# Kernel optimization log

Hardware: AMD Instinct MI355X
Metric: run time of the kernel (lower is better)

## Reference

```python
import jax, jax.numpy as jnp
import numpy as np

N, T = 4096, 1024
COND, PRED, PERIOD = 896, 56, 7


def setup_inputs() -> dict:
    key = jax.random.key(0)
    k1, k2 = jax.random.split(key)
    query = jax.random.normal(k1, (N, T), dtype=jnp.float32)
    # learned per-location params: [init_level, level_sm_logit, init_trend,
    #  trend_sm_logit, season_sm, period seasonality logits]
    params = 0.1 * jax.random.normal(k2, (N, 5 + PERIOD), dtype=jnp.float32)
    return {"query": query, "params": params}


def _forward(query, params):
    init_level = params[:, 0]                       # [N]
    level_sm = jax.nn.sigmoid(params[:, 1])         # [N]
    init_trend = params[:, 2]                       # [N]
    trend_sm = jax.nn.sigmoid(params[:, 3])         # [N]
    season_sm = params[:, 4]                        # NOTE: no sigmoid, matches original code
    init_seas = jax.nn.sigmoid(params[:, -PERIOD:])  # [N, PERIOD]

    def step(carry, y):
        prev_level, prev_trend, buf = carry          # buf: rolling window of last PERIOD seasonalities
        s_t = buf[:, 0]                              # seasonalities[t]
        pred = prev_level + prev_trend
        level = level_sm * y + (1.0 - level_sm) * pred
        diff = jnp.abs(level - prev_level)
        trend = trend_sm * (level - prev_level) + (1.0 - trend_sm) * prev_trend
        new_seas = season_sm * (y - pred) + (1.0 - season_sm) * s_t
        buf = jnp.concatenate([buf[:, 1:], new_seas[:, None]], axis=1)
        return (level, trend, buf), (level, trend, new_seas, diff)

    carry0 = (init_level, init_trend, init_seas)
    _, (levels, trends, new_seas_seq, diffs) = jax.lax.scan(step, carry0, query.T)
    levels = levels.T            # [N, T]
    trends = trends.T            # [N, T]
    new_seas_seq = new_seas_seq.T  # [N, T], == seasonalities[:, PERIOD:]
    level_diffs = diffs.T.mean(axis=1)  # [N]

    # full seasonality sequence: PERIOD initial values followed by T computed ones
    seas_full = jnp.concatenate([init_seas, new_seas_seq], axis=1)  # [N, PERIOD+T]

    sm = query - levels - new_seas_seq  # [N, T]

    horizon = jnp.arange(1, PRED + 1, dtype=levels.dtype)  # [PRED]
    last_levels = levels[:, COND - 1:, None]   # [N, W, 1], W = T-COND+1
    last_trends = trends[:, COND - 1:, None]
    pr = last_levels + last_trends * horizon   # [N, W, PRED]

    # cyclic seasonality forecast per window
    season_index = jnp.tile(jnp.arange(PERIOD), (PRED + PERIOD - 1) // PERIOD)[:PRED]
    starts = jnp.arange(COND, T + 1)           # [W]
    idx = starts[:, None] + season_index[None, :]  # [W, PRED]
    pr = pr + seas_full[:, idx]                # [N, W, PRED]

    return sm, pr, level_diffs


def reference(query, params):
    return _forward(query, params)
```

## Files before the change

kernel.cpp:

```cpp
#include <hip/hip_runtime.h>
#include <cmath>

#define NROWS 4096
#define TLEN  1024
#define RPB   8
#define LT0   895
#define ST0   889
#define LTN   129
#define STN   135
#define PRV4R 1806
#define PRV4B (RPB * PRV4R)

__device__ __forceinline__ float sigmoidf_(float x) {
    return 1.0f / (1.0f + expf(-x));
}

__device__ __forceinline__ float f4c(const float4& v, int k) {
    switch (k & 3) { case 0: return v.x; case 1: return v.y; case 2: return v.z; default: return v.w; }
}

__global__ __launch_bounds__(512, 4)
void es_fused(const float* __restrict__ query,
              const float* __restrict__ params,
              float* __restrict__ sm,
              float* __restrict__ diffs,
              float4* __restrict__ pr4)
{
    __shared__ float4 ystage[RPB * 256];
    __shared__ float lds_P[RPB * 65];
    __shared__ float lds_start[RPB * 65];
    __shared__ float lds_q[RPB * 225];
    __shared__ float lds_dsum[RPB * 33];
    __shared__ float lds_par[RPB * 16];
    __shared__ float Ltl[RPB * 132];
    __shared__ float Ttl[RPB * 132];
    __shared__ float Stl[RPB * 136];

    const int tid = threadIdx.x;
    const int base = blockIdx.x * RPB;
    const int r = (tid >> 5) & 7;
    const int k = tid & 31;
    const int n = base + r;

    {
        const float4* qb = reinterpret_cast<const float4*>(query + (size_t)base * TLEN);
        #pragma unroll
        for (int i = 0; i < 4; ++i) {
            const int w = i * 512 + tid;
            ystage[(w & ~7) | ((w ^ (w >> 3)) & 7)] = qb[w];
        }
    }

    float a = 0.f, b = 0.f, c = 0.f, ia = 0.f, ib = 0.f, ic = 0.f;
    if (tid < 256) {
        const float* pp = params + (size_t)n * 12;
        a  = sigmoidf_(pp[1]);
        b  = sigmoidf_(pp[3]);
        c  = pp[4];
        ia = 1.0f - a; ib = 1.0f - b; ic = 1.0f - c;
        if (k == 0) {
            float* par = &lds_par[r * 16];
            par[0] = pp[0];
            par[1] = pp[2];
            par[2] = ia;
            par[3] = -(a * b);
            par[4] = ib + b * ia;
            par[5] = ic;
            #pragma unroll
            for (int l = 0; l < 7; ++l) par[6 + l] = sigmoidf_(pp[5 + l]);
        }
    }
    __syncthreads();

    float4 yv[8];
    float e[32];
    float st0 = 0.f, st1 = 0.f;

    if (tid < 256) {
        const int ksw = k & 7;
        #pragma unroll
        for (int i = 0; i < 8; ++i)
            yv[i] = ystage[r * 256 + ((k * 8 + i) ^ ksw)];

        float L = 0.0f, B = 0.0f;
        #pragma unroll
        for (int j = 0; j < 32; ++j) {
            const float yy = f4c(yv[j >> 2], j);
            const float pred  = L + B;
            const float level = fmaf(a, yy, ia * pred);
            const float trend = fmaf(b, level - L, ib * B);
            L = level; B = trend;
        }
        lds_P[r * 65 + 2 * k]     = L;
        lds_P[r * 65 + 2 * k + 1] = B;
    }
    __syncthreads();

    if (tid < 8) {
        const float* par = &lds_par[tid * 16];
        float m00 = par[2], m01 = par[2], m10 = par[3], m11 = par[4];
        #pragma unroll
        for (int s = 0; s < 5; ++s) {
            const float t00 = m00 * m00 + m01 * m10;
            const float t01 = m00 * m01 + m01 * m11;
            const float t10 = m10 * m00 + m11 * m10;
            const float t11 = m10 * m01 + m11 * m11;
            m00 = t00; m01 = t01; m10 = t10; m11 = t11;
        }
        float P0[32], P1[32];
        #pragma unroll
        for (int kk = 0; kk < 32; ++kk) {
            P0[kk] = lds_P[tid * 65 + 2 * kk];
            P1[kk] = lds_P[tid * 65 + 2 * kk + 1];
        }
        float s0 = par[0], s1 = par[1];
        #pragma unroll
        for (int kk = 0; kk < 32; ++kk) {
            lds_start[tid * 65 + 2 * kk]     = s0;
            lds_start[tid * 65 + 2 * kk + 1] = s1;
            const float t0 = m00 * s0 + m01 * s1 + P0[kk];
            const float t1 = m10 * s0 + m11 * s1 + P1[kk];
            s0 = t0; s1 = t1;
        }
    }
    __syncthreads();

    if (tid < 256) {
        st0 = lds_start[r * 65 + 2 * k];
        st1 = lds_start[r * 65 + 2 * k + 1];
        float L = st0, B = st1, dsum = 0.0f;
        float q[7] = {0,0,0,0,0,0,0};
        #pragma unroll
        for (int j = 0; j < 32; ++j) {
            const float yy = f4c(yv[j >> 2], j);
            const float pred  = L + B;
            const float level = fmaf(a, yy, ia * pred);
            const float d     = level - L;
            dsum += fabsf(d);
            const float trend = fmaf(b, d, ib * B);
            const float ee    = yy - pred;
            e[j] = ee;
            q[j % 7] = fmaf(ic, q[j % 7], c * ee);
            L = level; B = trend;
        }
        const int kp = (4 * k) % 7;
        #pragma unroll
        for (int l = 0; l < 7; ++l) {
            int g = kp + l; if (g >= 7) g -= 7;
            lds_q[r * 225 + k * 7 + g] = q[l];
        }
        lds_dsum[r * 33 + k] = dsum;

        if (k >= 27) {
            float prevL = st0, Bv = st1;
            #pragma unroll
            for (int j = 0; j < 32; ++j) {
                const float level = f4c(yv[j >> 2], j) - ia * e[j];
                const float trend = fmaf(b, level - prevL, ib * Bv);
                const int tg = k * 32 + j;
                if (tg >= LT0) {
                    Ltl[r * 132 + tg - LT0] = level;
                    Ttl[r * 132 + tg - LT0] = trend;
                }
                prevL = level; Bv = trend;
            }
        }
    }
    __syncthreads();

    if (tid < 56) {
        const int rr = tid / 7, p = tid % 7;
        const float icc = lds_par[rr * 16 + 5];
        const float ic2 = icc * icc;
        const float ic4 = ic2 * ic2;
        const float ic5 = ic4 * icc;
        float v = lds_par[rr * 16 + 6 + p];
        float qq[32];
        #pragma unroll
        for (int kk = 0; kk < 32; ++kk) qq[kk] = lds_q[rr * 225 + kk * 7 + p];
        int l = p;
        #pragma unroll
        for (int kk = 0; kk < 32; ++kk) {
            const float m = (l < 4) ? ic5 : ic4;
            const float nv = fmaf(m, v, qq[kk]);
            lds_q[rr * 225 + kk * 7 + p] = v;
            v = nv;
            l += 3; if (l >= 7) l -= 7;
        }
    } else if (tid < 64) {
        const int rr = tid - 56;
        float s = 0.0f;
        #pragma unroll
        for (int kk = 0; kk < 32; ++kk) s += lds_dsum[rr * 33 + kk];
        diffs[blockIdx.x * RPB + rr] = s * (1.0f / 1024.0f);
    }
    __syncthreads();

    if (tid < 256) {
        float sg[7];
        const int kp = (4 * k) % 7;
        #pragma unroll
        for (int l = 0; l < 7; ++l) {
            int g = kp + l; if (g >= 7) g -= 7;
            sg[l] = lds_q[r * 225 + k * 7 + g];
        }
        const int ksw = k & 7;
        float4 ov;
        #pragma unroll
        for (int j = 0; j < 32; ++j) {
            const float sn = fmaf(ic, sg[j % 7], c * e[j]);
            sg[j % 7] = sn;
            const float smv = ia * e[j] - sn;
            e[j] = sn;
            switch (j & 3) { case 0: ov.x = smv; break; case 1: ov.y = smv; break;
                             case 2: ov.z = smv; break; default: ov.w = smv; }
            if ((j & 3) == 3)
                ystage[r * 256 + ((k * 8 + (j >> 2)) ^ ksw)] = ov;
        }
        if (k >= 27) {
            #pragma unroll
            for (int j = 0; j < 32; ++j) {
                const int tg = k * 32 + j;
                if (tg >= ST0) Stl[r * 136 + tg - ST0] = e[j];
            }
        }
    }
    __syncthreads();

    {
        float4* smb = reinterpret_cast<float4*>(sm + (size_t)base * TLEN);
        #pragma unroll
        for (int i = 0; i < 4; ++i) {
            const int w = i * 512 + tid;
            smb[w] = ystage[(w & ~7) | ((w ^ (w >> 3)) & 7)];
        }
    }

    {
        float4* prb = pr4 + (size_t)blockIdx.x * PRV4B;
        #pragma unroll 4
        for (int i = 0; i < 28; ++i) {
            const int q = i * 512 + tid;
            const int row = q / PRV4R;
            const int rem = q - row * PRV4R;
            const int s   = rem / 14;
            const int h4  = rem - s * 14;
            const float L = Ltl[row * 132 + s];
            const float T = Ttl[row * 132 + s];
            const float* stp = &Stl[row * 136 + s];
            const int hb = h4 * 4;
            int m0 = hb % 7;
            int m1 = m0 + 1; if (m1 >= 7) m1 -= 7;
            int m2 = m1 + 1; if (m2 >= 7) m2 -= 7;
            int m3 = m2 + 1; if (m3 >= 7) m3 -= 7;
            const float hbf = (float)hb;
            float4 o;
            o.x = fmaf(T, hbf + 1.0f, L) + stp[m0];
            o.y = fmaf(T, hbf + 2.0f, L) + stp[m1];
            o.z = fmaf(T, hbf + 3.0f, L) + stp[m2];
            o.w = fmaf(T, hbf + 4.0f, L) + stp[m3];
            prb[q] = o;
        }
        const int q = 28 * 512 + tid;
        if (q < PRV4B) {
            const int row = q / PRV4R;
            const int rem = q - row * PRV4R;
            const int s   = rem / 14;
            const int h4  = rem - s * 14;
            const float L = Ltl[row * 132 + s];
            const float T = Ttl[row * 132 + s];
            const float* stp = &Stl[row * 136 + s];
            const int hb = h4 * 4;
            int m0 = hb % 7;
            int m1 = m0 + 1; if (m1 >= 7) m1 -= 7;
            int m2 = m1 + 1; if (m2 >= 7) m2 -= 7;
            int m3 = m2 + 1; if (m3 >= 7) m3 -= 7;
            const float hbf = (float)hb;
            float4 o;
            o.x = fmaf(T, hbf + 1.0f, L) + stp[m0];
            o.y = fmaf(T, hbf + 2.0f, L) + stp[m1];
            o.z = fmaf(T, hbf + 3.0f, L) + stp[m2];
            o.w = fmaf(T, hbf + 4.0f, L) + stp[m3];
            prb[q] = o;
        }
    }
}

extern "C" void kernel_launch(void* const* d_in, const int* in_sizes, int n_in,
                              void* d_out, int out_size, void* d_ws, size_t ws_size,
                              hipStream_t stream) {
    const float* query  = (const float*)d_in[0];
    const float* params = (const float*)d_in[1];

    float* out   = (float*)d_out;
    float* sm    = out;
    float* pr    = out + (size_t)NROWS * TLEN;
    float* diffs = pr  + (size_t)NROWS * 129 * 56;

    hipLaunchKernelGGL(es_fused, dim3(NROWS / RPB), dim3(512), 0, stream,
                       query, params, sm, diffs, (float4*)pr);
}
```

Baseline: 34.77 us.

## Overlap sm writes with pr emission by splitting threads into specialized groups

Threads with k>=27 first compute only the seasonality tail needed for the pr forecast. After a barrier, the upper 256 threads start emitting pr while the lower 256 recompute the seasonal recurrence and write sm straight to global memory, then emit the rest of pr. This drops the LDS ystage staging pass and one barrier, so sm stores overlap pr stores. The cost is recomputing part of the recurrence and direct strided float4 sm stores that may coalesce worse than the old staged layout.

```diff
diff --git a/kernel.cpp b/kernel.cpp
--- a/kernel.cpp
+++ b/kernel.cpp
@@ -18,6 +18,30 @@
 __device__ __forceinline__ float f4c(const float4& v, int k) {
     switch (k & 3) { case 0: return v.x; case 1: return v.y; case 2: return v.z; default: return v.w; }
 }
+
+#define PR_EMIT(qv_)                                                          \
+    {                                                                         \
+        const int q_   = (qv_);                                               \
+        const int row_ = q_ / PRV4R;                                          \
+        const int rem_ = q_ - row_ * PRV4R;                                   \
+        const int s_   = rem_ / 14;                                           \
+        const int h4_  = rem_ - s_ * 14;                                      \
+        const float L_ = Ltl[row_ * 132 + s_];                                \
+        const float T_ = Ttl[row_ * 132 + s_];                                \
+        const float* stp_ = &Stl[row_ * 136 + s_];                            \
+        const int hb_ = h4_ * 4;                                              \
+        int m0_ = hb_ % 7;                                                    \
+        int m1_ = m0_ + 1; if (m1_ >= 7) m1_ -= 7;                            \
+        int m2_ = m1_ + 1; if (m2_ >= 7) m2_ -= 7;                            \
+        int m3_ = m2_ + 1; if (m3_ >= 7) m3_ -= 7;                            \
+        const float hbf_ = (float)hb_;                                        \
+        float4 o_;                                                            \
+        o_.x = fmaf(T_, hbf_ + 1.0f, L_) + stp_[m0_];                         \
+        o_.y = fmaf(T_, hbf_ + 2.0f, L_) + stp_[m1_];                         \
+        o_.z = fmaf(T_, hbf_ + 3.0f, L_) + stp_[m2_];                         \
+        o_.w = fmaf(T_, hbf_ + 4.0f, L_) + stp_[m3_];                         \
+        prb[q_] = o_;                                                         \
+    }
 
 __global__ __launch_bounds__(512, 4)
 void es_fused(const float* __restrict__ query,
@@ -196,7 +220,7 @@
     }
     __syncthreads();
 
-    if (tid < 256) {
+    if (tid < 256 && k >= 27) {
         float sg[7];
         const int kp = (4 * k) % 7;
         #pragma unroll
@@ -204,84 +228,52 @@
             int g = kp + l; if (g >= 7) g -= 7;
             sg[l] = lds_q[r * 225 + k * 7 + g];
         }
-        const int ksw = k & 7;
-        float4 ov;
         #pragma unroll
         for (int j = 0; j < 32; ++j) {
             const float sn = fmaf(ic, sg[j % 7], c * e[j]);
             sg[j % 7] = sn;
-            const float smv = ia * e[j] - sn;
-            e[j] = sn;
-            switch (j & 3) { case 0: ov.x = smv; break; case 1: ov.y = smv; break;
-                             case 2: ov.z = smv; break; default: ov.w = smv; }
-            if ((j & 3) == 3)
-                ystage[r * 256 + ((k * 8 + (j >> 2)) ^ ksw)] = ov;
-        }
-        if (k >= 27) {
+            const int tg = k * 32 + j;
+            if (tg >= ST0) Stl[r * 136 + tg - ST0] = sn;
+        }
+    }
+    __syncthreads();
+
+    float4* prb = pr4 + (size_t)blockIdx.x * PRV4B;
+
+    if (tid >= 256) {
+        const int u = tid - 256;
+        #pragma unroll 4
+        for (int i = 0; i < 32; ++i) {
+            PR_EMIT(i * 256 + u);
+        }
+    } else {
+        {
+            float sg[7];
+            const int kp = (4 * k) % 7;
+            #pragma unroll
+            for (int l = 0; l < 7; ++l) {
+                int g = kp + l; if (g >= 7) g -= 7;
+                sg[l] = lds_q[r * 225 + k * 7 + g];
+            }
+            float4 ov;
+            float* smrow = sm + (size_t)n * TLEN + k * 32;
             #pragma unroll
             for (int j = 0; j < 32; ++j) {
-                const int tg = k * 32 + j;
-                if (tg >= ST0) Stl[r * 136 + tg - ST0] = e[j];
+                const float sn = fmaf(ic, sg[j % 7], c * e[j]);
+                sg[j % 7] = sn;
+                const float smv = ia * e[j] - sn;
+                switch (j & 3) { case 0: ov.x = smv; break; case 1: ov.y = smv; break;
+                                 case 2: ov.z = smv; break; default: ov.w = smv; }
+                if ((j & 3) == 3)
+                    *reinterpret_cast<float4*>(smrow + (j - 3)) = ov;
             }
         }
-    }
-    __syncthreads();
-
-    {
-        float4* smb = reinterpret_cast<float4*>(sm + (size_t)base * TLEN);
-        #pragma unroll
-        for (int i = 0; i < 4; ++i) {
-            const int w = i * 512 + tid;
-            smb[w] = ystage[(w & ~7) | ((w ^ (w >> 3)) & 7)];
-        }
-    }
-
-    {
-        float4* prb = pr4 + (size_t)blockIdx.x * PRV4B;
         #pragma unroll 4
-        for (int i = 0; i < 28; ++i) {
-            const int q = i * 512 + tid;
-            const int row = q / PRV4R;
-            const int rem = q - row * PRV4R;
-            const int s   = rem / 14;
-            const int h4  = rem - s * 14;
-            const float L = Ltl[row * 132 + s];
-            const float T = Ttl[row * 132 + s];
-            const float* stp = &Stl[row * 136 + s];
-            const int hb = h4 * 4;
-            int m0 = hb % 7;
-            int m1 = m0 + 1; if (m1 >= 7) m1 -= 7;
-            int m2 = m1 + 1; if (m2 >= 7) m2 -= 7;
-            int m3 = m2 + 1; if (m3 >= 7) m3 -= 7;
-            const float hbf = (float)hb;
-            float4 o;
-            o.x = fmaf(T, hbf + 1.0f, L) + stp[m0];
-            o.y = fmaf(T, hbf + 2.0f, L) + stp[m1];
-            o.z = fmaf(T, hbf + 3.0f, L) + stp[m2];
-            o.w = fmaf(T, hbf + 4.0f, L) + stp[m3];
-            prb[q] = o;
-        }
-        const int q = 28 * 512 + tid;
-        if (q < PRV4B) {
-            const int row = q / PRV4R;
-            const int rem = q - row * PRV4R;
-            const int s   = rem / 14;
-            const int h4  = rem - s * 14;
-            const float L = Ltl[row * 132 + s];
-            const float T = Ttl[row * 132 + s];
-            const float* stp = &Stl[row * 136 + s];
-            const int hb = h4 * 4;
-            int m0 = hb % 7;
-            int m1 = m0 + 1; if (m1 >= 7) m1 -= 7;
-            int m2 = m1 + 1; if (m2 >= 7) m2 -= 7;
-            int m3 = m2 + 1; if (m3 >= 7) m3 -= 7;
-            const float hbf = (float)hb;
-            float4 o;
-            o.x = fmaf(T, hbf + 1.0f, L) + stp[m0];
-            o.y = fmaf(T, hbf + 2.0f, L) + stp[m1];
-            o.z = fmaf(T, hbf + 3.0f, L) + stp[m2];
-            o.w = fmaf(T, hbf + 4.0f, L) + stp[m3];
-            prb[q] = o;
+        for (int i = 0; i < 24; ++i) {
+            PR_EMIT(8192 + i * 256 + tid);
+        }
+        if (tid < 112) {
+            PR_EMIT(8192 + 6144 + tid);
         }
     }
 }
```

Measured after the change: 37.41 us. +7.6%, slower.

## Split forecast expansion into separate grid-wide kernel via workspace

Applied to the files above, without the earlier changes.

The fused kernel is split in two. The scan kernel now writes the per-row tail level, trend and seasonality tiles to a global workspace, and a second kernel with 4096 blocks of 256 threads expands them into the large pr output. Block indices in the scan kernel are also swizzled across rows. The aim is to spread the dominant pr store traffic over many more waves than the 512 scan blocks, at the cost of a second launch and a small extra workspace round trip.

```diff
diff --git a/kernel.cpp b/kernel.cpp
--- a/kernel.cpp
+++ b/kernel.cpp
@@ -6,10 +6,9 @@
 #define RPB   8
 #define LT0   895
 #define ST0   889
-#define LTN   129
-#define STN   135
 #define PRV4R 1806
-#define PRV4B (RPB * PRV4R)
+#define PRV4  (NROWS * PRV4R)
+#define NBB   4096
 
 __device__ __forceinline__ float sigmoidf_(float x) {
     return 1.0f / (1.0f + expf(-x));
@@ -20,11 +19,13 @@
 }
 
 __global__ __launch_bounds__(512, 4)
-void es_fused(const float* __restrict__ query,
-              const float* __restrict__ params,
-              float* __restrict__ sm,
-              float* __restrict__ diffs,
-              float4* __restrict__ pr4)
+void es_scan(const float* __restrict__ query,
+             const float* __restrict__ params,
+             float* __restrict__ sm,
+             float* __restrict__ diffs,
+             float* __restrict__ Ltg,
+             float* __restrict__ Ttg,
+             float* __restrict__ Stg)
 {
     __shared__ float4 ystage[RPB * 256];
     __shared__ float lds_P[RPB * 65];
@@ -37,7 +38,9 @@
     __shared__ float Stl[RPB * 136];
 
     const int tid = threadIdx.x;
-    const int base = blockIdx.x * RPB;
+    const int bid = blockIdx.x;
+    const int sw  = (bid & 7) * 64 + (bid >> 3);
+    const int base = sw * RPB;
     const int r = (tid >> 5) & 7;
     const int k = tid & 31;
     const int n = base + r;
@@ -192,7 +195,7 @@
         float s = 0.0f;
         #pragma unroll
         for (int kk = 0; kk < 32; ++kk) s += lds_dsum[rr * 33 + kk];
-        diffs[blockIdx.x * RPB + rr] = s * (1.0f / 1024.0f);
+        diffs[sw * RPB + rr] = s * (1.0f / 1024.0f);
     }
     __syncthreads();
 
@@ -237,17 +240,40 @@
     }
 
     {
-        float4* prb = pr4 + (size_t)blockIdx.x * PRV4B;
-        #pragma unroll 4
-        for (int i = 0; i < 28; ++i) {
-            const int q = i * 512 + tid;
-            const int row = q / PRV4R;
-            const int rem = q - row * PRV4R;
+        const float4* Lt4 = reinterpret_cast<const float4*>(Ltl);
+        const float4* Tt4 = reinterpret_cast<const float4*>(Ttl);
+        const float4* St4 = reinterpret_cast<const float4*>(Stl);
+        float4* Lg4 = reinterpret_cast<float4*>(Ltg + (size_t)base * 132);
+        float4* Tg4 = reinterpret_cast<float4*>(Ttg + (size_t)base * 132);
+        float4* Sg4 = reinterpret_cast<float4*>(Stg + (size_t)base * 136);
+        if (tid < 264) {
+            Lg4[tid] = Lt4[tid];
+            Tg4[tid] = Tt4[tid];
+        }
+        if (tid < 272) {
+            Sg4[tid] = St4[tid];
+        }
+    }
+}
+
+__global__ __launch_bounds__(256)
+void es_pr(const float* __restrict__ Ltg,
+           const float* __restrict__ Ttg,
+           const float* __restrict__ Stg,
+           float4* __restrict__ pr4)
+{
+    const int t0 = blockIdx.x * 256 + threadIdx.x;
+    #pragma unroll
+    for (int i = 0; i < 8; ++i) {
+        const int q = i * (NBB * 256) + t0;
+        if (q < PRV4) {
+            const int n   = q / PRV4R;
+            const int rem = q - n * PRV4R;
             const int s   = rem / 14;
             const int h4  = rem - s * 14;
-            const float L = Ltl[row * 132 + s];
-            const float T = Ttl[row * 132 + s];
-            const float* stp = &Stl[row * 136 + s];
+            const float L = Ltg[(size_t)n * 132 + s];
+            const float T = Ttg[(size_t)n * 132 + s];
+            const float* stp = Stg + (size_t)n * 136 + s;
             const int hb = h4 * 4;
             int m0 = hb % 7;
             int m1 = m0 + 1; if (m1 >= 7) m1 -= 7;
@@ -259,29 +285,7 @@
             o.y = fmaf(T, hbf + 2.0f, L) + stp[m1];
             o.z = fmaf(T, hbf + 3.0f, L) + stp[m2];
             o.w = fmaf(T, hbf + 4.0f, L) + stp[m3];
-            prb[q] = o;
-        }
-        const int q = 28 * 512 + tid;
-        if (q < PRV4B) {
-            const int row = q / PRV4R;
-            const int rem = q - row * PRV4R;
-            const int s   = rem / 14;
-            const int h4  = rem - s * 14;
-            const float L = Ltl[row * 132 + s];
-            const float T = Ttl[row * 132 + s];
-            const float* stp = &Stl[row * 136 + s];
-            const int hb = h4 * 4;
-            int m0 = hb % 7;
-            int m1 = m0 + 1; if (m1 >= 7) m1 -= 7;
-            int m2 = m1 + 1; if (m2 >= 7) m2 -= 7;
-            int m3 = m2 + 1; if (m3 >= 7) m3 -= 7;
-            const float hbf = (float)hb;
-            float4 o;
-            o.x = fmaf(T, hbf + 1.0f, L) + stp[m0];
-            o.y = fmaf(T, hbf + 2.0f, L) + stp[m1];
-            o.z = fmaf(T, hbf + 3.0f, L) + stp[m2];
-            o.w = fmaf(T, hbf + 4.0f, L) + stp[m3];
-            prb[q] = o;
+            pr4[q] = o;
         }
     }
 }
@@ -297,6 +301,12 @@
     float* pr    = out + (size_t)NROWS * TLEN;
     float* diffs = pr  + (size_t)NROWS * 129 * 56;
 
-    hipLaunchKernelGGL(es_fused, dim3(NROWS / RPB), dim3(512), 0, stream,
-                       query, params, sm, diffs, (float4*)pr);
-}
+    float* Ltg = (float*)d_ws;
+    float* Ttg = Ltg + (size_t)NROWS * 132;
+    float* Stg = Ttg + (size_t)NROWS * 132;
+
+    hipLaunchKernelGGL(es_scan, dim3(NROWS / RPB), dim3(512), 0, stream,
+                       query, params, sm, diffs, Ltg, Ttg, Stg);
+    hipLaunchKernelGGL(es_pr, dim3(NBB), dim3(256), 0, stream,
+                       Ltg, Ttg, Stg, (float4*)pr);
+}
```

New measurement: 43.84 us. +26.1%, slower.
